# Kernel tuning notes

Measured on AMD Instinct MI355X. Metric: run time of the kernel, lower is better.

## Reference

```python
import jax, jax.numpy as jnp
import numpy as np

B, L, D, H = 4, 4096, 2048, 128


def setup_inputs() -> dict:
    key = jax.random.key(0)
    k1, k2, k3, k4 = jax.random.split(key, 4)
    scale = 1.0 / np.sqrt(D)
    return {
        "x": jax.random.normal(k1, (B, L, D), dtype=jnp.float32),
        "Wq": jax.random.normal(k2, (D, H), dtype=jnp.float32) * scale,
        "Wk": jax.random.normal(k3, (D, H), dtype=jnp.float32) * scale,
        "Wv": jax.random.normal(k4, (D, H), dtype=jnp.float32) * scale,
    }


def reference(x, Wq, Wk, Wv):
    # single-head causal self-attention (dropout in eval mode / p=0)
    L_ = x.shape[1]
    q = jnp.einsum("bld,dh->blh", x, Wq)  # [B,L,H]
    k = jnp.einsum("bld,dh->blh", x, Wk)
    v = jnp.einsum("bld,dh->blh", x, Wv)
    scores = jnp.einsum("bqh,bkh->bqk", q, k) / jnp.sqrt(jnp.float32(q.shape[-1]))
    causal = jnp.tril(jnp.ones((L_, L_), dtype=bool))
    scores = jnp.where(causal, scores, -jnp.inf)
    probs = jax.nn.softmax(scores, axis=-1)
    return jnp.einsum("bqk,bkh->bqh", probs, v)
```

## Files before the change

kernel.cpp:

```cpp
#include <hip/hip_runtime.h>
#include <hip/hip_bf16.h>

#define B_ 4
#define L_ 4096
#define D_ 2048
#define H_ 128
#define M_ (B_ * L_)

typedef __attribute__((ext_vector_type(8))) short bf16x8;
typedef __attribute__((ext_vector_type(4))) float f32x4;
typedef __attribute__((ext_vector_type(16))) float f32x16;

__device__ __forceinline__ unsigned short f2bf(float f) {
  union { float f; unsigned u; } v; v.f = f;
  unsigned r = v.u + 0x7FFFu + ((v.u >> 16) & 1u);
  return (unsigned short)(r >> 16);
}

__device__ __forceinline__ unsigned cvt_pk_bf16(float lo, float hi) {
  unsigned r;
  asm("v_cvt_pk_bf16_f32 %0, %1, %2" : "=v"(r) : "v"(lo), "v"(hi));
  return r;
}

__device__ __forceinline__ void async_copy16(void* lds, const void* gptr) {
  __builtin_amdgcn_global_load_lds(
      (const __attribute__((address_space(1))) unsigned int*)gptr,
      (__attribute__((address_space(3))) unsigned int*)lds, 16, 0, 0);
}

__global__ void wconv(const float* __restrict__ Wq, const float* __restrict__ Wk,
                      const float* __restrict__ Wv, unsigned short* __restrict__ Wt) {
  int i = blockIdx.x * 256 + threadIdx.x;
  int m = i >> 18;
  int rem = i & 262143;
  int n = rem >> 11;
  int d = rem & 2047;
  const float* W = (m == 0) ? Wq : (m == 1 ? Wk : Wv);
  float val = W[(size_t)d * H_ + n];
  if (m == 0) val *= 0.08838834764831845f;
  Wt[(((size_t)(m << 7) + n) << 11) + d] = f2bf(val);
}

__global__ __launch_bounds__(256, 4) void qkv_gemm(
    const float* __restrict__ x, const unsigned short* __restrict__ Wt,
    unsigned short* __restrict__ qo, unsigned short* __restrict__ ko,
    unsigned short* __restrict__ vt) {
  __shared__ __align__(16) char Sm[32768];
  char* Ab = Sm;
  char* Bb = Sm + 16384;

  int bid = blockIdx.x;
  int xcd = bid & 7;
  int qq = bid >> 3;
  int mat = qq % 3;
  int rt = (qq / 3) * 8 + xcd;
  int row0 = rt * 64;

  int tid = threadIdx.x;
  int lane = tid & 63, w = tid >> 6;
  int wrow = (w >> 1) * 32;
  int wcol = (w & 1) * 64;
  int l15 = lane & 15, lhi = lane >> 4;

  f32x4 zero = {0.f, 0.f, 0.f, 0.f};
  f32x4 acc[2][4];
#pragma unroll
  for (int i = 0; i < 2; i++)
#pragma unroll
    for (int j = 0; j < 4; j++) acc[i][j] = zero;

  const char* xg = (const char*)x;
  const char* wg = (const char*)(Wt + ((size_t)mat << 7) * D_);

  for (int t = 0; t < 32; t++) {
    int k0 = t * 64;
#pragma unroll
    for (int p = 0; p < 4; p++) {
      int o = (p * 256 + tid) * 16;
      int r = o >> 8;
      int cb = (o & 255) ^ ((r & 7) << 4);
      async_copy16(Ab + o, xg + (((size_t)(row0 + r) * D_ + k0) << 2) + cb);
    }
#pragma unroll
    for (int p = 0; p < 4; p++) {
      int o = (p * 256 + tid) * 16;
      int r = o >> 7;
      int cb = (o & 127) ^ ((r & 7) << 4);
      async_copy16(Bb + o, wg + (((size_t)r * D_ + k0) << 1) + cb);
    }
    __syncthreads();

#pragma unroll
    for (int ks = 0; ks < 2; ks++) {
      bf16x8 af[2], bfr[4];
#pragma unroll
      for (int mi = 0; mi < 2; mi++) {
        int r = wrow + mi * 16 + l15;
        int sw = (r & 7) << 4;
        int cb = ks * 128 + lhi * 32;
        float4 lo = *(const float4*)(Ab + r * 256 + (cb ^ sw));
        float4 hi = *(const float4*)(Ab + r * 256 + ((cb + 16) ^ sw));
        union { bf16x8 v; unsigned u[4]; } tt;
        tt.u[0] = cvt_pk_bf16(lo.x, lo.y);
        tt.u[1] = cvt_pk_bf16(lo.z, lo.w);
        tt.u[2] = cvt_pk_bf16(hi.x, hi.y);
        tt.u[3] = cvt_pk_bf16(hi.z, hi.w);
        af[mi] = tt.v;
      }
#pragma unroll
      for (int ni = 0; ni < 4; ni++) {
        int r = wcol + ni * 16 + l15;
        int sw = (r & 7) << 4;
        int cb = ks * 64 + lhi * 16;
        bfr[ni] = *(const bf16x8*)(Bb + r * 128 + (cb ^ sw));
      }
#pragma unroll
      for (int mi = 0; mi < 2; mi++)
#pragma unroll
        for (int ni = 0; ni < 4; ni++)
          acc[mi][ni] = __builtin_amdgcn_mfma_f32_16x16x32_bf16(af[mi], bfr[ni], acc[mi][ni], 0, 0, 0);
    }
    __syncthreads();
  }

  if (mat < 2) {
    unsigned short* dst = (mat == 0) ? qo : ko;
#pragma unroll
    for (int mi = 0; mi < 2; mi++)
#pragma unroll
      for (int ni = 0; ni < 4; ni++)
#pragma unroll
        for (int r = 0; r < 4; r++) {
          int m = row0 + wrow + mi * 16 + lhi * 4 + r;
          int cc = wcol + ni * 16 + l15;
          dst[(size_t)m * H_ + cc] = f2bf(acc[mi][ni][r]);
        }
  } else {
    unsigned short* Tls = (unsigned short*)Sm + w * 2560;
#pragma unroll
    for (int ni = 0; ni < 4; ni++)
#pragma unroll
      for (int mi = 0; mi < 2; mi++)
#pragma unroll
        for (int r = 0; r < 4; r++)
          Tls[(ni * 16 + l15) * 40 + mi * 16 + lhi * 4 + r] = f2bf(acc[mi][ni][r]);
    int b = row0 >> 12;
    int Lbase = (row0 & 4095) + wrow;
    int h = wcol + lane;
#pragma unroll
    for (int j = 0; j < 4; j++) {
      bf16x8 v = *(const bf16x8*)&Tls[lane * 40 + j * 8];
      *(bf16x8*)&vt[(((size_t)(b * H_ + h)) << 12) + Lbase + j * 8] = v;
    }
  }
}

__global__ __launch_bounds__(256, 2) void attn(
    const unsigned short* __restrict__ q, const unsigned short* __restrict__ k,
    const unsigned short* __restrict__ vt, float* __restrict__ po,
    float* __restrict__ pm, float* __restrict__ pl) {
  __shared__ __align__(16) char Kb[2][16384];
  __shared__ __align__(16) char Vb[2][16384];

  int bid = blockIdx.x;
  int b = bid & 3;
  int p2 = bid >> 2;
  int j, c;
  if (p2 < 32)      { j = 31 - (p2 >> 2);            c = p2 & 3; }
  else if (p2 < 56) { int i = p2 - 32; int d3 = i / 3; j = 23 - d3; c = i - 3 * d3; }
  else if (p2 < 72) { int i = p2 - 56; j = 15 - (i >> 1); c = i & 1; }
  else              { j = 7 - (p2 - 72);             c = 0; }

  int kbase = c << 10;
  int kmax = min((c + 1) << 10, (j + 1) << 7);
  int NT = (kmax - kbase) >> 6;

  int tid = threadIdx.x;
  int w = tid >> 6, lane = tid & 63;
  int q31 = lane & 31, hi = lane >> 5;
  int qw0 = (j << 7) + (w << 5);
  int kcap = qw0 + 32;

  const unsigned short* qb = q + ((size_t)b << 12) * H_;
  const char* kbyte = (const char*)(k + ((size_t)b << 12) * H_);
  const char* vbyte = (const char*)(vt + ((size_t)b * H_ << 12));

  bf16x8 qf[8];
#pragma unroll
  for (int kk = 0; kk < 8; kk++)
    qf[kk] = *(const bf16x8*)&qb[(size_t)(qw0 + q31) * H_ + kk * 16 + hi * 8];

  f32x16 o[4];
#pragma unroll
  for (int hb = 0; hb < 4; hb++)
#pragma unroll
    for (int r = 0; r < 16; r++) o[hb][r] = 0.f;
  float mrun = -1e30f, lrun = 0.f;

  int ksw = (q31 & 7) << 4;

#define STAGE(bi, k0)                                                          \
  {                                                                            \
    _Pragma("unroll") for (int p = 0; p < 4; p++) {                            \
      int oo = (p * 256 + tid) * 16;                                           \
      int rr = oo >> 8;                                                        \
      int cc = (oo & 255) ^ ((rr & 7) << 4);                                   \
      async_copy16(Kb[bi] + oo, kbyte + (size_t)((k0) + rr) * 256 + cc);       \
    }                                                                          \
    _Pragma("unroll") for (int p = 0; p < 4; p++) {                            \
      int oo = (p * 256 + tid) * 16;                                           \
      int hh = oo >> 7;                                                        \
      int cc = (oo & 127) ^ ((hh & 7) << 4);                                   \
      async_copy16(Vb[bi] + oo, vbyte + (size_t)hh * 8192 + (size_t)(k0) * 2 + cc); \
    }                                                                          \
  }

  STAGE(0, kbase);

  for (int t = 0; t < NT; t++) {
    __syncthreads();
    int k0 = kbase + (t << 6);
    if (t + 1 < NT) STAGE((t + 1) & 1, k0 + 64);
    const char* Kc = Kb[t & 1];
    const char* Vc = Vb[t & 1];

#pragma unroll
    for (int sub = 0; sub < 2; sub++) {
      int k0s = k0 + (sub << 5);
      if (k0s < kcap) {
        int kloc2 = sub << 5;
        const char* Krow = Kc + (kloc2 + q31) * 256;
        f32x16 s;
#pragma unroll
        for (int r = 0; r < 16; r++) s[r] = 0.f;
#pragma unroll
        for (int kk = 0; kk < 8; kk++) {
          bf16x8 kf = *(const bf16x8*)(Krow + ((kk * 32 + hi * 16) ^ ksw));
          s = __builtin_amdgcn_mfma_f32_32x32x16_bf16(kf, qf[kk], s, 0, 0, 0);
        }
        if (k0s == qw0) {
#pragma unroll
          for (int r = 0; r < 16; r++) {
            int kloc = (r & 3) + 8 * (r >> 2) + 4 * hi;
            if (kloc > q31) s[r] = -1e30f;
          }
        }
        float m0 = fmaxf(fmaxf(s[0], s[1]), fmaxf(s[2], s[3]));
        float m1 = fmaxf(fmaxf(s[4], s[5]), fmaxf(s[6], s[7]));
        float m2 = fmaxf(fmaxf(s[8], s[9]), fmaxf(s[10], s[11]));
        float m3 = fmaxf(fmaxf(s[12], s[13]), fmaxf(s[14], s[15]));
        float mt = fmaxf(fmaxf(m0, m1), fmaxf(m2, m3));
        mt = fmaxf(mt, __shfl_xor(mt, 32, 64));
        if (!__all(mt <= mrun + 8.f)) {
          float mn = fmaxf(mrun, mt);
          float al = __expf(mrun - mn);
          mrun = mn;
          lrun *= al;
#pragma unroll
          for (int hb = 0; hb < 4; hb++)
#pragma unroll
            for (int r = 0; r < 16; r++) o[hb][r] *= al;
        }
        float p[16], ls = 0.f;
#pragma unroll
        for (int r = 0; r < 16; r++) {
          p[r] = __expf(s[r] - mrun);
          ls += p[r];
        }
        ls += __shfl_xor(ls, 32, 64);
        lrun += ls;
        unsigned c0 = cvt_pk_bf16(p[0], p[1]),   c1 = cvt_pk_bf16(p[2], p[3]);
        unsigned c2 = cvt_pk_bf16(p[4], p[5]),   c3 = cvt_pk_bf16(p[6], p[7]);
        unsigned c4 = cvt_pk_bf16(p[8], p[9]),   c5 = cvt_pk_bf16(p[10], p[11]);
        unsigned c6 = cvt_pk_bf16(p[12], p[13]), c7 = cvt_pk_bf16(p[14], p[15]);
        unsigned e0 = (unsigned)__shfl_xor((int)(hi ? c0 : c2), 32, 64);
        unsigned e1 = (unsigned)__shfl_xor((int)(hi ? c1 : c3), 32, 64);
        unsigned e2 = (unsigned)__shfl_xor((int)(hi ? c4 : c6), 32, 64);
        unsigned e3 = (unsigned)__shfl_xor((int)(hi ? c5 : c7), 32, 64);
        union { unsigned u[4]; bf16x8 v; } pb0, pb1;
        pb0.u[0] = hi ? e0 : c0; pb0.u[1] = hi ? e1 : c1;
        pb0.u[2] = hi ? c2 : e0; pb0.u[3] = hi ? c3 : e1;
        pb1.u[0] = hi ? e2 : c4; pb1.u[1] = hi ? e3 : c5;
        pb1.u[2] = hi ? c6 : e2; pb1.u[3] = hi ? c7 : e3;
#pragma unroll
        for (int hb = 0; hb < 4; hb++) {
          const char* Vrow = Vc + (hb * 32 + q31) * 128;
          bf16x8 v0 = *(const bf16x8*)(Vrow + ((kloc2 * 2 + hi * 16) ^ ksw));
          bf16x8 v1 = *(const bf16x8*)(Vrow + ((kloc2 * 2 + 32 + hi * 16) ^ ksw));
          o[hb] = __builtin_amdgcn_mfma_f32_32x32x16_bf16(v0, pb0.v, o[hb], 0, 0, 0);
          o[hb] = __builtin_amdgcn_mfma_f32_32x32x16_bf16(v1, pb1.v, o[hb], 0, 0, 0);
        }
      }
    }
  }
#undef STAGE

  int qtile = (j << 2) + w;
  int slot = (((b << 7) + qtile) << 2) + c;
  float* pob = po + ((size_t)slot << 12);
#pragma unroll
  for (int hb = 0; hb < 4; hb++)
#pragma unroll
    for (int rq = 0; rq < 4; rq++) {
      float4 v;
      v.x = o[hb][rq * 4 + 0];
      v.y = o[hb][rq * 4 + 1];
      v.z = o[hb][rq * 4 + 2];
      v.w = o[hb][rq * 4 + 3];
      *(float4*)&pob[q31 * 128 + 32 * hb + 8 * rq + 4 * hi] = v;
    }
  if (lane < 32) {
    pm[slot * 32 + q31] = mrun;
    pl[slot * 32 + q31] = lrun;
  }
}

__global__ __launch_bounds__(256) void combine(
    const float* __restrict__ po, const float* __restrict__ pm,
    const float* __restrict__ pl, float* __restrict__ out) {
  int bid = blockIdx.x;
  int b = bid >> 7, t = bid & 127;
  int nc = (((t + 1) << 5) + 1023) >> 10;
  int tid = threadIdx.x;
  int row = tid >> 3;
  int hb = (tid & 7) << 4;
  int base = bid * 4;

  float M = -1e30f;
  for (int ci = 0; ci < nc; ci++) M = fmaxf(M, pm[(base + ci) * 32 + row]);
  float L = 0.f;
  float a[16];
#pragma unroll
  for (int j = 0; j < 16; j++) a[j] = 0.f;
  for (int ci = 0; ci < nc; ci++) {
    int sl = base + ci;
    float wgt = __expf(pm[sl * 32 + row] - M);
    L += pl[sl * 32 + row] * wgt;
    const float* p = po + ((size_t)sl << 12) + row * 128 + hb;
#pragma unroll
    for (int j = 0; j < 4; j++) {
      float4 v = *(const float4*)(p + j * 4);
      a[j * 4 + 0] += v.x * wgt;
      a[j * 4 + 1] += v.y * wgt;
      a[j * 4 + 2] += v.z * wgt;
      a[j * 4 + 3] += v.w * wgt;
    }
  }
  float inv = 1.f / L;
  float* ob = out + ((size_t)((b << 12) + (t << 5) + row)) * 128 + hb;
#pragma unroll
  for (int j = 0; j < 16; j++) ob[j] = a[j] * inv;
}

extern "C" void kernel_launch(void* const* d_in, const int* in_sizes, int n_in,
                              void* d_out, int out_size, void* d_ws, size_t ws_size,
                              hipStream_t stream) {
  const float* x  = (const float*)d_in[0];
  const float* Wq = (const float*)d_in[1];
  const float* Wk = (const float*)d_in[2];
  const float* Wv = (const float*)d_in[3];

  unsigned short* ws = (unsigned short*)d_ws;
  unsigned short* Wt = ws;
  unsigned short* qo = ws + 786432;
  unsigned short* ko = qo + (size_t)M_ * H_;
  unsigned short* vt = ko + (size_t)M_ * H_;
  float* po = (float*)(vt + (size_t)M_ * H_);
  float* pm = po + (size_t)2048 * 4096;
  float* pl = pm + 2048 * 32;
  float* out = (float*)d_out;

  hipLaunchKernelGGL(wconv, dim3(3072), dim3(256), 0, stream, Wq, Wk, Wv, Wt);
  hipLaunchKernelGGL(qkv_gemm, dim3(768), dim3(256), 0, stream, x, Wt, qo, ko, vt);
  hipLaunchKernelGGL(attn, dim3(320), dim3(256), 0, stream, qo, ko, vt, po, pm, pl);
  hipLaunchKernelGGL(combine, dim3(512), dim3(256), 0, stream, po, pm, pl, out);
}
```

Baseline: 281.4 us.

## Double-buffer QKV GEMM with register-staged bf16 A, split attention finer with bf16 partials

The QKV GEMM now loads x through registers, converts it to bf16 before writing LDS, and double-buffers both A and B tiles, so the next tile's loads overlap the current MFMAs and the x tile in LDS is half the size. Attention splits the key range into 512-wide chunks instead of 1024, raising the grid from 320 to 576 blocks for better CU occupancy and balance. Partial outputs are stored as bf16 to halve partial-buffer traffic, and combine reads up to 8 chunks. The risks are more combine work, extra rounding of the partials, and a larger workspace.

```diff
diff --git a/kernel.cpp b/kernel.cpp
--- a/kernel.cpp
+++ b/kernel.cpp
@@ -21,6 +21,13 @@
   unsigned r;
   asm("v_cvt_pk_bf16_f32 %0, %1, %2" : "=v"(r) : "v"(lo), "v"(hi));
   return r;
+}
+
+__device__ __forceinline__ float bf_lo(unsigned u) {
+  union { unsigned x; float f; } t; t.x = u << 16; return t.f;
+}
+__device__ __forceinline__ float bf_hi(unsigned u) {
+  union { unsigned x; float f; } t; t.x = u & 0xFFFF0000u; return t.f;
 }
 
 __device__ __forceinline__ void async_copy16(void* lds, const void* gptr) {
@@ -46,9 +53,7 @@
     const float* __restrict__ x, const unsigned short* __restrict__ Wt,
     unsigned short* __restrict__ qo, unsigned short* __restrict__ ko,
     unsigned short* __restrict__ vt) {
-  __shared__ __align__(16) char Sm[32768];
-  char* Ab = Sm;
-  char* Bb = Sm + 16384;
+  __shared__ __align__(16) char Sm[49152];
 
   int bid = blockIdx.x;
   int xcd = bid & 7;
@@ -70,50 +75,63 @@
 #pragma unroll
     for (int j = 0; j < 4; j++) acc[i][j] = zero;
 
-  const char* xg = (const char*)x;
   const char* wg = (const char*)(Wt + ((size_t)mat << 7) * D_);
 
+  int ar = tid >> 2;
+  int acb = (tid & 3) << 5;
+  int asw = (ar & 7) << 4;
+  const float* xga = x + (size_t)(row0 + ar) * D_ + ((tid & 3) << 4);
+
+#define QSTAGE_B(bi, k0)                                                       \
+  _Pragma("unroll") for (int p = 0; p < 4; p++) {                              \
+    int o = (p * 256 + tid) * 16;                                              \
+    int r = o >> 7;                                                            \
+    int cb = (o & 127) ^ ((r & 7) << 4);                                       \
+    async_copy16(Sm + 16384 + (bi) * 16384 + o,                                \
+                 wg + (((size_t)r * D_ + (k0)) << 1) + cb);                    \
+  }
+
+  {
+    float4 av[4];
+#pragma unroll
+    for (int j = 0; j < 4; j++) av[j] = *(const float4*)(xga + j * 4);
+    QSTAGE_B(0, 0);
+    unsigned u[8];
+#pragma unroll
+    for (int j = 0; j < 4; j++) {
+      u[2 * j] = cvt_pk_bf16(av[j].x, av[j].y);
+      u[2 * j + 1] = cvt_pk_bf16(av[j].z, av[j].w);
+    }
+    char* abase = Sm + ar * 128;
+    *(uint4*)(abase + (acb ^ asw)) = make_uint4(u[0], u[1], u[2], u[3]);
+    *(uint4*)(abase + ((acb + 16) ^ asw)) = make_uint4(u[4], u[5], u[6], u[7]);
+  }
+  __syncthreads();
+
   for (int t = 0; t < 32; t++) {
-    int k0 = t * 64;
-#pragma unroll
-    for (int p = 0; p < 4; p++) {
-      int o = (p * 256 + tid) * 16;
-      int r = o >> 8;
-      int cb = (o & 255) ^ ((r & 7) << 4);
-      async_copy16(Ab + o, xg + (((size_t)(row0 + r) * D_ + k0) << 2) + cb);
-    }
-#pragma unroll
-    for (int p = 0; p < 4; p++) {
-      int o = (p * 256 + tid) * 16;
-      int r = o >> 7;
-      int cb = (o & 127) ^ ((r & 7) << 4);
-      async_copy16(Bb + o, wg + (((size_t)r * D_ + k0) << 1) + cb);
-    }
-    __syncthreads();
-
+    int cur = t & 1, nxt = cur ^ 1;
+    bool hn = (t < 31);
+    float4 av[4];
+    if (hn) {
+      int k0n = (t + 1) * 64;
+#pragma unroll
+      for (int j = 0; j < 4; j++) av[j] = *(const float4*)(xga + k0n + j * 4);
+      QSTAGE_B(nxt, k0n);
+    }
+    const char* A = Sm + cur * 8192;
+    const char* Bp = Sm + 16384 + cur * 16384;
 #pragma unroll
     for (int ks = 0; ks < 2; ks++) {
       bf16x8 af[2], bfr[4];
 #pragma unroll
       for (int mi = 0; mi < 2; mi++) {
         int r = wrow + mi * 16 + l15;
-        int sw = (r & 7) << 4;
-        int cb = ks * 128 + lhi * 32;
-        float4 lo = *(const float4*)(Ab + r * 256 + (cb ^ sw));
-        float4 hi = *(const float4*)(Ab + r * 256 + ((cb + 16) ^ sw));
-        union { bf16x8 v; unsigned u[4]; } tt;
-        tt.u[0] = cvt_pk_bf16(lo.x, lo.y);
-        tt.u[1] = cvt_pk_bf16(lo.z, lo.w);
-        tt.u[2] = cvt_pk_bf16(hi.x, hi.y);
-        tt.u[3] = cvt_pk_bf16(hi.z, hi.w);
-        af[mi] = tt.v;
+        af[mi] = *(const bf16x8*)(A + r * 128 + ((ks * 64 + lhi * 16) ^ ((r & 7) << 4)));
       }
 #pragma unroll
       for (int ni = 0; ni < 4; ni++) {
         int r = wcol + ni * 16 + l15;
-        int sw = (r & 7) << 4;
-        int cb = ks * 64 + lhi * 16;
-        bfr[ni] = *(const bf16x8*)(Bb + r * 128 + (cb ^ sw));
+        bfr[ni] = *(const bf16x8*)(Bp + r * 128 + ((ks * 64 + lhi * 16) ^ ((r & 7) << 4)));
       }
 #pragma unroll
       for (int mi = 0; mi < 2; mi++)
@@ -121,8 +139,20 @@
         for (int ni = 0; ni < 4; ni++)
           acc[mi][ni] = __builtin_amdgcn_mfma_f32_16x16x32_bf16(af[mi], bfr[ni], acc[mi][ni], 0, 0, 0);
     }
+    if (hn) {
+      unsigned u[8];
+#pragma unroll
+      for (int j = 0; j < 4; j++) {
+        u[2 * j] = cvt_pk_bf16(av[j].x, av[j].y);
+        u[2 * j + 1] = cvt_pk_bf16(av[j].z, av[j].w);
+      }
+      char* abase = Sm + nxt * 8192 + ar * 128;
+      *(uint4*)(abase + (acb ^ asw)) = make_uint4(u[0], u[1], u[2], u[3]);
+      *(uint4*)(abase + ((acb + 16) ^ asw)) = make_uint4(u[4], u[5], u[6], u[7]);
+    }
     __syncthreads();
   }
+#undef QSTAGE_B
 
   if (mat < 2) {
     unsigned short* dst = (mat == 0) ? qo : ko;
@@ -158,23 +188,21 @@
 
 __global__ __launch_bounds__(256, 2) void attn(
     const unsigned short* __restrict__ q, const unsigned short* __restrict__ k,
-    const unsigned short* __restrict__ vt, float* __restrict__ po,
+    const unsigned short* __restrict__ vt, unsigned short* __restrict__ po,
     float* __restrict__ pm, float* __restrict__ pl) {
   __shared__ __align__(16) char Kb[2][16384];
   __shared__ __align__(16) char Vb[2][16384];
 
   int bid = blockIdx.x;
   int b = bid & 3;
-  int p2 = bid >> 2;
-  int j, c;
-  if (p2 < 32)      { j = 31 - (p2 >> 2);            c = p2 & 3; }
-  else if (p2 < 56) { int i = p2 - 32; int d3 = i / 3; j = 23 - d3; c = i - 3 * d3; }
-  else if (p2 < 72) { int i = p2 - 56; j = 15 - (i >> 1); c = i & 1; }
-  else              { j = 7 - (p2 - 72);             c = 0; }
-
-  int kbase = c << 10;
-  int kmax = min((c + 1) << 10, (j + 1) << 7);
-  int NT = (kmax - kbase) >> 6;
+  int p = bid >> 2;
+  int c = 0;
+  while (p >= 32 - 4 * c) { p -= 32 - 4 * c; c++; }
+  int j = 31 - p;
+
+  int kbase = c << 9;
+  int kmax = min((c + 1) << 9, (j + 1) << 7);
+  int NT = (kmax - kbase + 63) >> 6;
 
   int tid = threadIdx.x;
   int w = tid >> 6, lane = tid & 63;
@@ -202,14 +230,14 @@
 
 #define STAGE(bi, k0)                                                          \
   {                                                                            \
-    _Pragma("unroll") for (int p = 0; p < 4; p++) {                            \
-      int oo = (p * 256 + tid) * 16;                                           \
+    _Pragma("unroll") for (int pp = 0; pp < 4; pp++) {                         \
+      int oo = (pp * 256 + tid) * 16;                                          \
       int rr = oo >> 8;                                                        \
       int cc = (oo & 255) ^ ((rr & 7) << 4);                                   \
       async_copy16(Kb[bi] + oo, kbyte + (size_t)((k0) + rr) * 256 + cc);       \
     }                                                                          \
-    _Pragma("unroll") for (int p = 0; p < 4; p++) {                            \
-      int oo = (p * 256 + tid) * 16;                                           \
+    _Pragma("unroll") for (int pp = 0; pp < 4; pp++) {                         \
+      int oo = (pp * 256 + tid) * 16;                                          \
       int hh = oo >> 7;                                                        \
       int cc = (oo & 127) ^ ((hh & 7) << 4);                                   \
       async_copy16(Vb[bi] + oo, vbyte + (size_t)hh * 8192 + (size_t)(k0) * 2 + cc); \
@@ -262,18 +290,18 @@
 #pragma unroll
             for (int r = 0; r < 16; r++) o[hb][r] *= al;
         }
-        float p[16], ls = 0.f;
+        float pp[16], ls = 0.f;
 #pragma unroll
         for (int r = 0; r < 16; r++) {
-          p[r] = __expf(s[r] - mrun);
-          ls += p[r];
+          pp[r] = __expf(s[r] - mrun);
+          ls += pp[r];
         }
         ls += __shfl_xor(ls, 32, 64);
         lrun += ls;
-        unsigned c0 = cvt_pk_bf16(p[0], p[1]),   c1 = cvt_pk_bf16(p[2], p[3]);
-        unsigned c2 = cvt_pk_bf16(p[4], p[5]),   c3 = cvt_pk_bf16(p[6], p[7]);
-        unsigned c4 = cvt_pk_bf16(p[8], p[9]),   c5 = cvt_pk_bf16(p[10], p[11]);
-        unsigned c6 = cvt_pk_bf16(p[12], p[13]), c7 = cvt_pk_bf16(p[14], p[15]);
+        unsigned c0 = cvt_pk_bf16(pp[0], pp[1]),   c1 = cvt_pk_bf16(pp[2], pp[3]);
+        unsigned c2 = cvt_pk_bf16(pp[4], pp[5]),   c3 = cvt_pk_bf16(pp[6], pp[7]);
+        unsigned c4 = cvt_pk_bf16(pp[8], pp[9]),   c5 = cvt_pk_bf16(pp[10], pp[11]);
+        unsigned c6 = cvt_pk_bf16(pp[12], pp[13]), c7 = cvt_pk_bf16(pp[14], pp[15]);
         unsigned e0 = (unsigned)__shfl_xor((int)(hi ? c0 : c2), 32, 64);
         unsigned e1 = (unsigned)__shfl_xor((int)(hi ? c1 : c3), 32, 64);
         unsigned e2 = (unsigned)__shfl_xor((int)(hi ? c4 : c6), 32, 64);
@@ -297,18 +325,15 @@
 #undef STAGE
 
   int qtile = (j << 2) + w;
-  int slot = (((b << 7) + qtile) << 2) + c;
-  float* pob = po + ((size_t)slot << 12);
+  int slot = (((b << 7) + qtile) << 3) + c;
+  unsigned short* pob = po + ((size_t)slot << 12);
 #pragma unroll
   for (int hb = 0; hb < 4; hb++)
 #pragma unroll
     for (int rq = 0; rq < 4; rq++) {
-      float4 v;
-      v.x = o[hb][rq * 4 + 0];
-      v.y = o[hb][rq * 4 + 1];
-      v.z = o[hb][rq * 4 + 2];
-      v.w = o[hb][rq * 4 + 3];
-      *(float4*)&pob[q31 * 128 + 32 * hb + 8 * rq + 4 * hi] = v;
+      unsigned u0 = cvt_pk_bf16(o[hb][rq * 4 + 0], o[hb][rq * 4 + 1]);
+      unsigned u1 = cvt_pk_bf16(o[hb][rq * 4 + 2], o[hb][rq * 4 + 3]);
+      *(uint2*)&pob[q31 * 128 + 32 * hb + 8 * rq + 4 * hi] = make_uint2(u0, u1);
     }
   if (lane < 32) {
     pm[slot * 32 + q31] = mrun;
@@ -317,15 +342,15 @@
 }
 
 __global__ __launch_bounds__(256) void combine(
-    const float* __restrict__ po, const float* __restrict__ pm,
+    const unsigned short* __restrict__ po, const float* __restrict__ pm,
     const float* __restrict__ pl, float* __restrict__ out) {
   int bid = blockIdx.x;
   int b = bid >> 7, t = bid & 127;
-  int nc = (((t + 1) << 5) + 1023) >> 10;
+  int nc = (t + 16) >> 4;
   int tid = threadIdx.x;
   int row = tid >> 3;
   int hb = (tid & 7) << 4;
-  int base = bid * 4;
+  int base = bid * 8;
 
   float M = -1e30f;
   for (int ci = 0; ci < nc; ci++) M = fmaxf(M, pm[(base + ci) * 32 + row]);
@@ -337,14 +362,14 @@
     int sl = base + ci;
     float wgt = __expf(pm[sl * 32 + row] - M);
     L += pl[sl * 32 + row] * wgt;
-    const float* p = po + ((size_t)sl << 12) + row * 128 + hb;
-#pragma unroll
-    for (int j = 0; j < 4; j++) {
-      float4 v = *(const float4*)(p + j * 4);
-      a[j * 4 + 0] += v.x * wgt;
-      a[j * 4 + 1] += v.y * wgt;
-      a[j * 4 + 2] += v.z * wgt;
-      a[j * 4 + 3] += v.w * wgt;
+    const unsigned short* p = po + ((size_t)sl << 12) + row * 128 + hb;
+    uint4 v0 = *(const uint4*)p;
+    uint4 v1 = *(const uint4*)(p + 8);
+    unsigned vv[8] = {v0.x, v0.y, v0.z, v0.w, v1.x, v1.y, v1.z, v1.w};
+#pragma unroll
+    for (int j = 0; j < 8; j++) {
+      a[j * 2 + 0] += bf_lo(vv[j]) * wgt;
+      a[j * 2 + 1] += bf_hi(vv[j]) * wgt;
     }
   }
   float inv = 1.f / L;
@@ -366,13 +391,13 @@
   unsigned short* qo = ws + 786432;
   unsigned short* ko = qo + (size_t)M_ * H_;
   unsigned short* vt = ko + (size_t)M_ * H_;
-  float* po = (float*)(vt + (size_t)M_ * H_);
-  float* pm = po + (size_t)2048 * 4096;
-  float* pl = pm + 2048 * 32;
+  unsigned short* po = vt + (size_t)M_ * H_;
+  float* pm = (float*)(po + (size_t)4096 * 4096);
+  float* pl = pm + 4096 * 32;
   float* out = (float*)d_out;
 
   hipLaunchKernelGGL(wconv, dim3(3072), dim3(256), 0, stream, Wq, Wk, Wv, Wt);
   hipLaunchKernelGGL(qkv_gemm, dim3(768), dim3(256), 0, stream, x, Wt, qo, ko, vt);
-  hipLaunchKernelGGL(attn, dim3(320), dim3(256), 0, stream, qo, ko, vt, po, pm, pl);
+  hipLaunchKernelGGL(attn, dim3(576), dim3(256), 0, stream, qo, ko, vt, po, pm, pl);
   hipLaunchKernelGGL(combine, dim3(512), dim3(256), 0, stream, po, pm, pl, out);
 }
```

Result: no change. 279.2 us (-0.8%).
